# Kernel tuning notes

Measured on AMD Instinct MI355X. Metric: run time of the kernel, lower is better.

The kernel has to match this reference:

```python
import jax, jax.numpy as jnp
import numpy as np

EPS = 1e-5

def layernorm(x, scale, bias):
    mu = jnp.mean(x, axis=-1, keepdims=True)
    var = jnp.var(x, axis=-1, keepdims=True)
    return (x - mu) * jax.lax.rsqrt(var + EPS) * scale + bias

def setup_inputs() -> dict:
    key = jax.random.key(0)
    ks = jax.random.split(key, 12)
    B, N, c_s, c_z, H = 1, 1024, 768, 128, 12
    sc = 1.0 / np.sqrt(c_s)
    inp = {
        "s": jax.random.normal(ks[0], (B, N, c_s), jnp.float32),
        "z": jax.random.normal(ks[1], (B, N, N, c_z), jnp.float32),
        "mask": jnp.ones((B, N), jnp.float32),
        "norm_s_scale": jnp.ones((c_s,), jnp.float32),
        "norm_s_bias": jnp.zeros((c_s,), jnp.float32),
        "Wq": jax.random.normal(ks[2], (c_s, c_s), jnp.float32) * sc,
        "bq": jax.random.normal(ks[3], (c_s,), jnp.float32) * 0.02,
        "Wk": jax.random.normal(ks[4], (c_s, c_s), jnp.float32) * sc,
        "Wv": jax.random.normal(ks[5], (c_s, c_s), jnp.float32) * sc,
        "Wg": jax.random.normal(ks[6], (c_s, c_s), jnp.float32) * sc,
        "norm_z_scale": jnp.ones((c_z,), jnp.float32),
        "norm_z_bias": jnp.zeros((c_z,), jnp.float32),
        "Wz": jax.random.normal(ks[7], (c_z, H), jnp.float32) / np.sqrt(c_z),
        "Wo": jax.random.normal(ks[8], (c_s, c_s), jnp.float32) * sc,  # zero-init in orig; random for nontrivial test
    }
    return inp

def reference(s, z, mask, norm_s_scale, norm_s_bias, Wq, bq, Wk, Wv, Wg,
              norm_z_scale, norm_z_bias, Wz, Wo):
    B, N, c_s = s.shape
    H = Wz.shape[1]
    D = c_s // H
    INF = 1000000.0
    sn = layernorm(s, norm_s_scale, norm_s_bias)                 # (B,N,c_s)
    q = (sn @ Wq + bq).reshape(B, N, H, D)
    k = (sn @ Wk).reshape(B, N, H, D)
    v = (sn @ Wv).reshape(B, N, H, D)
    g = jax.nn.sigmoid(sn @ Wg)                                  # (B,N,c_s)
    zb = jnp.einsum('bijc,ch->bhij', layernorm(z, norm_z_scale, norm_z_bias), Wz)
    attn = jnp.einsum('bihd,bjhd->bhij', q, k) / np.sqrt(D) + zb
    attn = attn + (1.0 - mask[:, None, None, :]) * -INF
    attn = jax.nn.softmax(attn, axis=-1)
    o = jnp.einsum('bhij,bjhd->bihd', attn, v).reshape(B, N, c_s)
    return (g * o) @ Wo
```

## Files before the change

kernel.cpp:

```cpp
#include <hip/hip_runtime.h>
#include <hip/hip_bf16.h>

#define CS 768
#define NTOK 1024
#define CZ 128
#define NH 12
#define HD 64
#define JC 8
#define SMAX_SHIFT 16.0f

typedef __attribute__((ext_vector_type(8))) short bf16x8;
typedef __attribute__((ext_vector_type(4))) float f32x4;
typedef __attribute__((ext_vector_type(8))) unsigned short ushort8_t;
typedef __attribute__((ext_vector_type(4))) unsigned short ushort4_t;

__device__ inline unsigned short f2bf(float f) {
  __hip_bfloat16 h = __float2bfloat16(f);
  return *reinterpret_cast<unsigned short*>(&h);
}
__device__ inline float bf2f(unsigned short u) {
  union { unsigned int i; float f; } c; c.i = ((unsigned int)u) << 16;
  return c.f;
}
__device__ inline unsigned int cvtpk_bf16(float lo, float hi) {
  unsigned int r;
  asm("v_cvt_pk_bf16_f32 %0, %1, %2" : "=v"(r) : "v"(lo), "v"(hi));
  return r;
}

__global__ __launch_bounds__(256) void prep_kernel(const float* __restrict__ s,
    const float* __restrict__ sc, const float* __restrict__ bi, unsigned short* __restrict__ sn,
    const float* __restrict__ W0, const float* __restrict__ W1, const float* __restrict__ W2,
    const float* __restrict__ W3, const float* __restrict__ W4, unsigned short* __restrict__ wt) {
  __shared__ float tile[64][65];
  int tid = threadIdx.x;
  if (blockIdx.x < NTOK) {
    int row = blockIdx.x;
    const float* x = s + (size_t)row * CS;
    float v0 = x[tid], v1 = x[tid + 256], v2 = x[tid + 512];
    float sum = v0 + v1 + v2;
    float sq  = v0*v0 + v1*v1 + v2*v2;
    for (int off = 1; off < 64; off <<= 1) {
      sum += __shfl_xor(sum, off);
      sq  += __shfl_xor(sq,  off);
    }
    __shared__ float ws1[4], ws2[4];
    if ((tid & 63) == 0) { ws1[tid >> 6] = sum; ws2[tid >> 6] = sq; }
    __syncthreads();
    float S = ws1[0] + ws1[1] + ws1[2] + ws1[3];
    float Q = ws2[0] + ws2[1] + ws2[2] + ws2[3];
    float mu  = S * (1.f / CS);
    float var = Q * (1.f / CS) - mu * mu;
    float rs  = rsqrtf(var + 1e-5f);
    unsigned short* y = sn + (size_t)row * CS;
    y[tid]       = f2bf((v0 - mu) * rs * sc[tid]       + bi[tid]);
    y[tid + 256] = f2bf((v1 - mu) * rs * sc[tid + 256] + bi[tid + 256]);
    y[tid + 512] = f2bf((v2 - mu) * rs * sc[tid + 512] + bi[tid + 512]);
  } else {
    int bz = blockIdx.x - NTOK;
    int w = bz / 144, rem = bz % 144;
    int kt = rem % 12, nt = rem / 12;
    const float* W = w == 0 ? W0 : w == 1 ? W1 : w == 2 ? W2 : w == 3 ? W3 : W4;
    unsigned short* Wt = wt + (size_t)w * CS * CS;
    int k0 = kt * 64, n0 = nt * 64;
    #pragma unroll
    for (int it = 0; it < 4; ++it) {
      int r = (tid >> 4) + it * 16;
      int c = (tid & 15) * 4;
      float4 vv = *(const float4*)(W + (size_t)(k0 + r) * CS + n0 + c);
      tile[r][c] = vv.x; tile[r][c+1] = vv.y; tile[r][c+2] = vv.z; tile[r][c+3] = vv.w;
    }
    __syncthreads();
    #pragma unroll
    for (int it = 0; it < 2; ++it) {
      int idx = tid + it * 256;
      int n = idx >> 3, k8 = (idx & 7) * 8;
      ushort8_t o;
      #pragma unroll
      for (int e = 0; e < 8; ++e) o[e] = f2bf(tile[k8 + e][n]);
      *(ushort8_t*)(Wt + (size_t)(n0 + n) * CS + k0 + k8) = o;
    }
  }
}

__global__ __launch_bounds__(256) void zbqkvg_kernel(const float* __restrict__ z,
    const float* __restrict__ gs, const float* __restrict__ gb,
    const float* __restrict__ Wz, const float* __restrict__ mask, float* __restrict__ zbuf,
    const unsigned short* __restrict__ A, const unsigned short* __restrict__ Wt,
    const float* __restrict__ bq, unsigned short* __restrict__ qb,
    unsigned short* __restrict__ kb, unsigned short* __restrict__ vtb,
    unsigned short* __restrict__ gbuf) {
  __shared__ __align__(16) unsigned short As[64][40];
  __shared__ __align__(16) unsigned short Bs[64][40];
  int tid = threadIdx.x;
  int bq11 = blockIdx.x / 11, br11 = blockIdx.x % 11;
  if (br11 < 8) {
    const int zbid = bq11 * 8 + br11;
    const int lane = tid & 63;
    const int il = lane & 15;
    const int qg = lane >> 4;
    const size_t NPAIR = (size_t)NTOK * NTOK;
    bf16x8 whi[4], wlo[4];
    float bh = 0.f;
    #pragma unroll
    for (int m = 0; m < 4; ++m) {
      union { unsigned short u[8]; bf16x8 v; } hi, lo;
      #pragma unroll
      for (int e = 0; e < 8; ++e) {
        int c = 32 * m + 8 * qg + e;
        float wv = (il < NH) ? Wz[c * NH + il] : 0.f;
        bh = fmaf(gb[c], wv, bh);
        float wp = gs[c] * wv;
        unsigned short h = f2bf(wp);
        hi.u[e] = h;
        lo.u[e] = f2bf(wp - bf2f(h));
      }
      whi[m] = hi.v; wlo[m] = lo.v;
    }
    bh += __shfl_xor(bh, 16);
    bh += __shfl_xor(bh, 32);

    const int wave = zbid * 4 + (tid >> 6);
    const int nWaves = 2048 * 4;
    for (size_t p0 = (size_t)wave * 16; p0 < NPAIR; p0 += (size_t)nWaves * 16) {
      const float* zrow = z + (p0 + il) * CZ;
      float zv[32];
      #pragma unroll
      for (int m = 0; m < 4; ++m) {
        float4 a = *(const float4*)(zrow + 32 * m + 8 * qg);
        float4 b = *(const float4*)(zrow + 32 * m + 8 * qg + 4);
        zv[m*8+0] = a.x; zv[m*8+1] = a.y; zv[m*8+2] = a.z; zv[m*8+3] = a.w;
        zv[m*8+4] = b.x; zv[m*8+5] = b.y; zv[m*8+6] = b.z; zv[m*8+7] = b.w;
      }
      float sum = 0.f, sq = 0.f;
      #pragma unroll
      for (int e = 0; e < 32; ++e) { sum += zv[e]; sq = fmaf(zv[e], zv[e], sq); }
      sum += __shfl_xor(sum, 16); sum += __shfl_xor(sum, 32);
      sq  += __shfl_xor(sq,  16); sq  += __shfl_xor(sq,  32);
      float mu  = sum * (1.f / CZ);
      float var = sq * (1.f / CZ) - mu * mu;
      float rs  = rsqrtf(var + 1e-5f);
      float nmr = -mu * rs;
      f32x4 acc = {};
      #pragma unroll
      for (int m = 0; m < 4; ++m) {
        union { unsigned int u[4]; bf16x8 v; } hi;
        #pragma unroll
        for (int e2 = 0; e2 < 4; ++e2) {
          float n0 = fmaf(zv[m*8+e2*2],     rs, nmr);
          float n1 = fmaf(zv[m*8+e2*2 + 1], rs, nmr);
          hi.u[e2] = cvtpk_bf16(n0, n1);
        }
        acc = __builtin_amdgcn_mfma_f32_16x16x32_bf16(hi.v, whi[m], acc, 0, 0, 0);
        acc = __builtin_amdgcn_mfma_f32_16x16x32_bf16(hi.v, wlo[m], acc, 0, 0, 0);
      }
      if (il < NH) {
        int j0 = (int)(p0 & (NTOK - 1)) + 4 * qg;
        float4 mk = *(const float4*)(mask + j0);
        float4 o;
        o.x = (acc[0] + bh + (1.f - mk.x) * -1000000.0f) * 1.44269504f - SMAX_SHIFT;
        o.y = (acc[1] + bh + (1.f - mk.y) * -1000000.0f) * 1.44269504f - SMAX_SHIFT;
        o.z = (acc[2] + bh + (1.f - mk.z) * -1000000.0f) * 1.44269504f - SMAX_SHIFT;
        o.w = (acc[3] + bh + (1.f - mk.w) * -1000000.0f) * 1.44269504f - SMAX_SHIFT;
        *(float4*)(zbuf + (size_t)il * NPAIR + p0 + 4 * qg) = o;
      }
    }
  } else {
    int bx = bq11 * 3 + (br11 - 8);
    int wid = tid >> 6, lane = tid & 63;
    int lrow = lane & 15, lk8 = (lane >> 4) * 8;
    int row0 = (bx / 48) * 64, col0 = (bx % 48) * 64;
    int ar = tid >> 2, ak = (tid & 3) * 8;
    f32x4 acc[4] = {};
    for (int k0 = 0; k0 < CS; k0 += 32) {
      *(ushort8_t*)&As[ar][ak] = *(const ushort8_t*)(A  + (size_t)(row0 + ar) * CS + k0 + ak);
      *(ushort8_t*)&Bs[ar][ak] = *(const ushort8_t*)(Wt + (size_t)(col0 + ar) * CS + k0 + ak);
      __syncthreads();
      bf16x8 af = *(bf16x8*)&As[wid * 16 + lrow][lk8];
      #pragma unroll
      for (int nb = 0; nb < 4; ++nb) {
        bf16x8 bfr = *(bf16x8*)&Bs[nb * 16 + lrow][lk8];
        acc[nb] = __builtin_amdgcn_mfma_f32_16x16x32_bf16(af, bfr, acc[nb], 0, 0, 0);
      }
      __syncthreads();
    }
    int sect = col0 / CS;
    int ncol0 = col0 - sect * CS;
    int grow0 = row0 + wid * 16 + (lane >> 4) * 4;
    if (sect == 2) {
      int jperm0 = ((grow0 >> 5) << 5) + 8 * (lane >> 4) + 4 * (wid & 1);
      #pragma unroll
      for (int nb = 0; nb < 4; ++nb) {
        int dg = ncol0 + nb * 16 + lrow;
        ushort4_t o;
        #pragma unroll
        for (int r = 0; r < 4; ++r) o[r] = f2bf(acc[nb][r]);
        *(ushort4_t*)(vtb + (size_t)dg * NTOK + jperm0) = o;
      }
    } else {
      unsigned short* dst = sect == 0 ? qb : sect == 1 ? kb : gbuf;
      #pragma unroll
      for (int nb = 0; nb < 4; ++nb) {
        int gcol = ncol0 + nb * 16 + lrow;
        float bv = (sect == 0) ? bq[gcol] : 0.f;
        #pragma unroll
        for (int r = 0; r < 4; ++r) {
          float val = acc[nb][r] + bv;
          if (sect == 3) val = 1.f / (1.f + __expf(-val));
          dst[(size_t)(grow0 + r) * CS + gcol] = f2bf(val);
        }
      }
    }
  }
}

__global__ __launch_bounds__(256) void flash_part(
    const unsigned short* __restrict__ qb, const unsigned short* __restrict__ kb,
    const unsigned short* __restrict__ vtb, const float* __restrict__ zbuf,
    float* __restrict__ Opart, float* __restrict__ lsum) {
  const int h = blockIdx.x;
  const int i0 = blockIdx.y * 64;
  const int jc = blockIdx.z;
  const int w = threadIdx.x >> 6, lane = threadIdx.x & 63;
  const int il = lane & 15, g = lane >> 4;
  const int irow = i0 + w * 16 + il;
  const float QKS = 0.125f * 1.44269504f;

  bf16x8 qf0 = *(const bf16x8*)(qb + (size_t)irow * CS + h * HD + g * 8);
  bf16x8 qf1 = *(const bf16x8*)(qb + (size_t)irow * CS + h * HD + 32 + g * 8);

  f32x4 oacc[4] = {};
  float plocal = 0.f;
  const float* zrow = zbuf + ((size_t)h << 20) + ((size_t)irow << 10);

  const int jlo = jc * (NTOK / JC), jhi = jlo + (NTOK / JC);
  for (int j0 = jlo; j0 < jhi; j0 += 64) {
    f32x4 sacc[4] = {};
    #pragma unroll
    for (int jb = 0; jb < 4; ++jb) {
      const unsigned short* kbase = kb + (size_t)(j0 + jb * 16 + il) * CS + h * HD;
      bf16x8 kf0 = *(const bf16x8*)(kbase + g * 8);
      bf16x8 kf1 = *(const bf16x8*)(kbase + 32 + g * 8);
      sacc[jb] = __builtin_amdgcn_mfma_f32_16x16x32_bf16(kf0, qf0, sacc[jb], 0, 0, 0);
      sacc[jb] = __builtin_amdgcn_mfma_f32_16x16x32_bf16(kf1, qf1, sacc[jb], 0, 0, 0);
    }
    unsigned int c0[4], c1[4];
    #pragma unroll
    for (int jb = 0; jb < 4; ++jb) {
      float4 z4 = *(const float4*)(zrow + j0 + jb * 16 + g * 4);
      float p0 = exp2f(fmaf(sacc[jb][0], QKS, z4.x));
      float p1 = exp2f(fmaf(sacc[jb][1], QKS, z4.y));
      float p2 = exp2f(fmaf(sacc[jb][2], QKS, z4.z));
      float p3 = exp2f(fmaf(sacc[jb][3], QKS, z4.w));
      plocal += (p0 + p1) + (p2 + p3);
      c0[jb] = cvtpk_bf16(p0, p1);
      c1[jb] = cvtpk_bf16(p2, p3);
    }
    #pragma unroll
    for (int js = 0; js < 2; ++js) {
      union { unsigned int u[4]; bf16x8 v; } pb;
      pb.u[0] = c0[2*js];
      pb.u[1] = c1[2*js];
      pb.u[2] = c0[2*js + 1];
      pb.u[3] = c1[2*js + 1];
      #pragma unroll
      for (int db = 0; db < 4; ++db) {
        bf16x8 vf = *(const bf16x8*)(vtb + (size_t)(h * HD + db * 16 + il) * NTOK + j0 + js * 32 + g * 8);
        oacc[db] = __builtin_amdgcn_mfma_f32_16x16x32_bf16(vf, pb.v, oacc[db], 0, 0, 0);
      }
    }
  }
  plocal += __shfl_xor(plocal, 16);
  plocal += __shfl_xor(plocal, 32);
  float* obase = Opart + ((size_t)(jc * NH + h) << 16) + ((size_t)irow << 6);
  #pragma unroll
  for (int db = 0; db < 4; ++db)
    *(float4*)(obase + db * 16 + g * 4) = *(float4*)&oacc[db];
  if (g == 0)
    lsum[((jc * NH + h) << 10) + irow] = plocal;
}

__global__ __launch_bounds__(256) void combine_kernel(const float* __restrict__ Opart,
    const float* __restrict__ lsum, const unsigned short* __restrict__ gbuf,
    unsigned short* __restrict__ gob) {
  int t = threadIdx.x;
  int r = blockIdx.x * 4 + (t >> 6);
  int h = r >> 10, i = r & (NTOK - 1), d = t & 63;
  float ltot = 0.f;
  #pragma unroll
  for (int c = 0; c < JC; ++c) ltot += lsum[((c * NH + h) << 10) + i];
  float o = 0.f;
  #pragma unroll
  for (int c = 0; c < JC; ++c)
    o += Opart[((size_t)(c * NH + h) << 16) + ((size_t)i << 6) + d];
  float inv = 1.f / ltot;
  size_t off = (size_t)i * CS + h * HD + d;
  gob[off] = f2bf(o * inv * bf2f(gbuf[off]));
}

__global__ __launch_bounds__(256) void out_gemm(const unsigned short* __restrict__ A,
    const unsigned short* __restrict__ Bt, float* __restrict__ C) {
  __shared__ __align__(16) unsigned short As[64][40];
  __shared__ __align__(16) unsigned short Bs[64][40];
  int tid = threadIdx.x;
  int wid = tid >> 6, lane = tid & 63;
  int lrow = lane & 15, lk8 = (lane >> 4) * 8;
  int row0 = blockIdx.y * 64, col0 = blockIdx.x * 64;
  int ar = tid >> 2, ak = (tid & 3) * 8;
  f32x4 acc[4] = {};
  for (int k0 = 0; k0 < CS; k0 += 32) {
    *(ushort8_t*)&As[ar][ak] = *(const ushort8_t*)(A  + (size_t)(row0 + ar) * CS + k0 + ak);
    *(ushort8_t*)&Bs[ar][ak] = *(const ushort8_t*)(Bt + (size_t)(col0 + ar) * CS + k0 + ak);
    __syncthreads();
    bf16x8 af = *(bf16x8*)&As[wid * 16 + lrow][lk8];
    #pragma unroll
    for (int nb = 0; nb < 4; ++nb) {
      bf16x8 bfr = *(bf16x8*)&Bs[nb * 16 + lrow][lk8];
      acc[nb] = __builtin_amdgcn_mfma_f32_16x16x32_bf16(af, bfr, acc[nb], 0, 0, 0);
    }
    __syncthreads();
  }
  #pragma unroll
  for (int nb = 0; nb < 4; ++nb) {
    int gcol = col0 + nb * 16 + lrow;
    #pragma unroll
    for (int r = 0; r < 4; ++r) {
      int grow = row0 + wid * 16 + (lane >> 4) * 4 + r;
      C[(size_t)grow * CS + gcol] = acc[nb][r];
    }
  }
}

extern "C" void kernel_launch(void* const* d_in, const int* in_sizes, int n_in,
                              void* d_out, int out_size, void* d_ws, size_t ws_size,
                              hipStream_t stream) {
  const float* s    = (const float*)d_in[0];
  const float* z    = (const float*)d_in[1];
  const float* mask = (const float*)d_in[2];
  const float* nss  = (const float*)d_in[3];
  const float* nsb  = (const float*)d_in[4];
  const float* Wq   = (const float*)d_in[5];
  const float* bq   = (const float*)d_in[6];
  const float* Wk   = (const float*)d_in[7];
  const float* Wv   = (const float*)d_in[8];
  const float* Wg   = (const float*)d_in[9];
  const float* nzs  = (const float*)d_in[10];
  const float* nzb  = (const float*)d_in[11];
  const float* Wz   = (const float*)d_in[12];
  const float* Wo   = (const float*)d_in[13];
  float* out = (float*)d_out;

  const size_t SN = (size_t)NTOK * CS;
  const size_t NPAIR = (size_t)NTOK * NTOK;
  const size_t WSZ = (size_t)CS * CS;

  float* zbuf  = (float*)d_ws;
  float* Opart = zbuf + NH * NPAIR;
  float* lsum  = Opart + (size_t)JC * NH * NTOK * HD;
  unsigned short* sn  = (unsigned short*)(lsum + (size_t)JC * NH * NTOK);
  unsigned short* qb  = sn  + SN;
  unsigned short* kb  = qb  + SN;
  unsigned short* vtb = kb  + SN;
  unsigned short* gbuf= vtb + SN;
  unsigned short* gob = gbuf+ SN;
  unsigned short* wt  = gob + SN;

  prep_kernel<<<NTOK + 720, 256, 0, stream>>>(s, nss, nsb, sn, Wq, Wk, Wv, Wg, Wo, wt);
  zbqkvg_kernel<<<2816, 256, 0, stream>>>(z, nzs, nzb, Wz, mask, zbuf,
                                          sn, wt, bq, qb, kb, vtb, gbuf);
  flash_part<<<dim3(NH, 16, JC), 256, 0, stream>>>(qb, kb, vtb, zbuf, Opart, lsum);
  combine_kernel<<<NH * NTOK / 4, 256, 0, stream>>>(Opart, lsum, gbuf, gob);
  out_gemm<<<dim3(12, 16), 256, 0, stream>>>(gob, wt + 4 * WSZ, out);
}
```

Before: 203.0 us.

## Fuse z layernorm pair bias into flash attention via fp16 shared memory tiles

Splits the QKVG GEMM back into its own kernel and fuses the z-projection (layernorm plus Wz MFMA) into the flash-attention kernel. Each block computes the pair bias for a 16x128 tile of all 12 heads into fp16 shared memory, then runs attention over that tile. This removes the 48MB fp32 zbuf write and re-read through HBM. In exchange the bias is stored in fp16, which loses precision, and the fused kernel runs on only 512 blocks with about 52KB of LDS each, so occupancy is lower. Overlap between the z pass and the GEMM in the old combined launch is also lost.

Result: faster. 176.1 us (median of 3 runs) (-13.3%).

```diff
diff --git a/kernel.cpp b/kernel.cpp
--- a/kernel.cpp
+++ b/kernel.cpp
@@ -1,5 +1,6 @@
 #include <hip/hip_runtime.h>
 #include <hip/hip_bf16.h>
+#include <hip/hip_fp16.h>
 
 #define CS 768
 #define NTOK 1024
@@ -7,7 +8,7 @@
 #define NH 12
 #define HD 64
 #define JC 8
-#define SMAX_SHIFT 16.0f
+#define ZHS 2184
 
 typedef __attribute__((ext_vector_type(8))) short bf16x8;
 typedef __attribute__((ext_vector_type(4))) float f32x4;
@@ -25,6 +26,11 @@
 __device__ inline unsigned int cvtpk_bf16(float lo, float hi) {
   unsigned int r;
   asm("v_cvt_pk_bf16_f32 %0, %1, %2" : "=v"(r) : "v"(lo), "v"(hi));
+  return r;
+}
+__device__ inline unsigned int cvtpk_f16(float lo, float hi) {
+  unsigned int r;
+  asm("v_cvt_pkrtz_f16_f32 %0, %1, %2" : "=v"(r) : "v"(lo), "v"(hi));
   return r;
 }
 
@@ -83,201 +89,201 @@
   }
 }
 
-__global__ __launch_bounds__(256) void zbqkvg_kernel(const float* __restrict__ z,
-    const float* __restrict__ gs, const float* __restrict__ gb,
-    const float* __restrict__ Wz, const float* __restrict__ mask, float* __restrict__ zbuf,
-    const unsigned short* __restrict__ A, const unsigned short* __restrict__ Wt,
-    const float* __restrict__ bq, unsigned short* __restrict__ qb,
-    unsigned short* __restrict__ kb, unsigned short* __restrict__ vtb,
-    unsigned short* __restrict__ gbuf) {
+__global__ __launch_bounds__(256) void qkvg_gemm(const unsigned short* __restrict__ A,
+    const unsigned short* __restrict__ Wt, const float* __restrict__ bq,
+    unsigned short* __restrict__ qb, unsigned short* __restrict__ kb,
+    unsigned short* __restrict__ vtb, unsigned short* __restrict__ gbuf) {
   __shared__ __align__(16) unsigned short As[64][40];
   __shared__ __align__(16) unsigned short Bs[64][40];
   int tid = threadIdx.x;
-  int bq11 = blockIdx.x / 11, br11 = blockIdx.x % 11;
-  if (br11 < 8) {
-    const int zbid = bq11 * 8 + br11;
-    const int lane = tid & 63;
-    const int il = lane & 15;
-    const int qg = lane >> 4;
-    const size_t NPAIR = (size_t)NTOK * NTOK;
-    bf16x8 whi[4], wlo[4];
-    float bh = 0.f;
+  int wid = tid >> 6, lane = tid & 63;
+  int lrow = lane & 15, lk8 = (lane >> 4) * 8;
+  int row0 = blockIdx.y * 64, col0 = blockIdx.x * 64;
+  int ar = tid >> 2, ak = (tid & 3) * 8;
+  f32x4 acc[4] = {};
+  for (int k0 = 0; k0 < CS; k0 += 32) {
+    *(ushort8_t*)&As[ar][ak] = *(const ushort8_t*)(A  + (size_t)(row0 + ar) * CS + k0 + ak);
+    *(ushort8_t*)&Bs[ar][ak] = *(const ushort8_t*)(Wt + (size_t)(col0 + ar) * CS + k0 + ak);
+    __syncthreads();
+    bf16x8 af = *(bf16x8*)&As[wid * 16 + lrow][lk8];
+    #pragma unroll
+    for (int nb = 0; nb < 4; ++nb) {
+      bf16x8 bfr = *(bf16x8*)&Bs[nb * 16 + lrow][lk8];
+      acc[nb] = __builtin_amdgcn_mfma_f32_16x16x32_bf16(af, bfr, acc[nb], 0, 0, 0);
+    }
+    __syncthreads();
+  }
+  int sect = col0 / CS;
+  int ncol0 = col0 - sect * CS;
+  int grow0 = row0 + wid * 16 + (lane >> 4) * 4;
+  if (sect == 2) {
+    int jperm0 = ((grow0 >> 5) << 5) + 8 * (lane >> 4) + 4 * (wid & 1);
+    #pragma unroll
+    for (int nb = 0; nb < 4; ++nb) {
+      int dg = ncol0 + nb * 16 + lrow;
+      ushort4_t o;
+      #pragma unroll
+      for (int r = 0; r < 4; ++r) o[r] = f2bf(acc[nb][r]);
+      *(ushort4_t*)(vtb + (size_t)dg * NTOK + jperm0) = o;
+    }
+  } else {
+    unsigned short* dst = sect == 0 ? qb : sect == 1 ? kb : gbuf;
+    #pragma unroll
+    for (int nb = 0; nb < 4; ++nb) {
+      int gcol = ncol0 + nb * 16 + lrow;
+      float bv = (sect == 0) ? bq[gcol] : 0.f;
+      #pragma unroll
+      for (int r = 0; r < 4; ++r) {
+        float val = acc[nb][r] + bv;
+        if (sect == 3) val = 1.f / (1.f + __expf(-val));
+        dst[(size_t)(grow0 + r) * CS + gcol] = f2bf(val);
+      }
+    }
+  }
+}
+
+__global__ __launch_bounds__(256) void zbflash_kernel(const float* __restrict__ z,
+    const float* __restrict__ gs, const float* __restrict__ gb,
+    const float* __restrict__ Wz, const float* __restrict__ mask,
+    const unsigned short* __restrict__ qb, const unsigned short* __restrict__ kb,
+    const unsigned short* __restrict__ vtb,
+    float* __restrict__ Opart, float* __restrict__ lsum) {
+  __shared__ __half zs[NH * ZHS];
+  const int i0 = blockIdx.x * 16;
+  const int jc = blockIdx.y;
+  const int j0 = jc * 128;
+  const int tid = threadIdx.x;
+  const int w = tid >> 6, lane = tid & 63;
+  const int il = lane & 15, qg = lane >> 4;
+  const float QKS = 0.125f * 1.44269504f;
+
+  bf16x8 whi[4], wlo[4];
+  float bh = 0.f;
+  #pragma unroll
+  for (int m = 0; m < 4; ++m) {
+    union { unsigned short u[8]; bf16x8 v; } hi, lo;
+    #pragma unroll
+    for (int e = 0; e < 8; ++e) {
+      int c = 32 * m + 8 * qg + e;
+      float wv = (il < NH) ? Wz[c * NH + il] : 0.f;
+      bh = fmaf(gb[c], wv, bh);
+      float wp = gs[c] * wv;
+      unsigned short h = f2bf(wp);
+      hi.u[e] = h;
+      lo.u[e] = f2bf(wp - bf2f(h));
+    }
+    whi[m] = hi.v; wlo[m] = lo.v;
+  }
+  bh += __shfl_xor(bh, 16);
+  bh += __shfl_xor(bh, 32);
+
+  for (int it = 0; it < 32; ++it) {
+    int group = w * 32 + it;
+    int i_local = group >> 3;
+    int jseg = group & 7;
+    const float* zrow = z + ((size_t)(i0 + i_local) * NTOK + j0 + jseg * 16 + il) * CZ;
+    float zv[32];
     #pragma unroll
     for (int m = 0; m < 4; ++m) {
-      union { unsigned short u[8]; bf16x8 v; } hi, lo;
-      #pragma unroll
-      for (int e = 0; e < 8; ++e) {
-        int c = 32 * m + 8 * qg + e;
-        float wv = (il < NH) ? Wz[c * NH + il] : 0.f;
-        bh = fmaf(gb[c], wv, bh);
-        float wp = gs[c] * wv;
-        unsigned short h = f2bf(wp);
-        hi.u[e] = h;
-        lo.u[e] = f2bf(wp - bf2f(h));
-      }
-      whi[m] = hi.v; wlo[m] = lo.v;
-    }
-    bh += __shfl_xor(bh, 16);
-    bh += __shfl_xor(bh, 32);
-
-    const int wave = zbid * 4 + (tid >> 6);
-    const int nWaves = 2048 * 4;
-    for (size_t p0 = (size_t)wave * 16; p0 < NPAIR; p0 += (size_t)nWaves * 16) {
-      const float* zrow = z + (p0 + il) * CZ;
-      float zv[32];
-      #pragma unroll
-      for (int m = 0; m < 4; ++m) {
-        float4 a = *(const float4*)(zrow + 32 * m + 8 * qg);
-        float4 b = *(const float4*)(zrow + 32 * m + 8 * qg + 4);
-        zv[m*8+0] = a.x; zv[m*8+1] = a.y; zv[m*8+2] = a.z; zv[m*8+3] = a.w;
-        zv[m*8+4] = b.x; zv[m*8+5] = b.y; zv[m*8+6] = b.z; zv[m*8+7] = b.w;
-      }
-      float sum = 0.f, sq = 0.f;
-      #pragma unroll
-      for (int e = 0; e < 32; ++e) { sum += zv[e]; sq = fmaf(zv[e], zv[e], sq); }
-      sum += __shfl_xor(sum, 16); sum += __shfl_xor(sum, 32);
-      sq  += __shfl_xor(sq,  16); sq  += __shfl_xor(sq,  32);
-      float mu  = sum * (1.f / CZ);
-      float var = sq * (1.f / CZ) - mu * mu;
-      float rs  = rsqrtf(var + 1e-5f);
-      float nmr = -mu * rs;
-      f32x4 acc = {};
-      #pragma unroll
-      for (int m = 0; m < 4; ++m) {
-        union { unsigned int u[4]; bf16x8 v; } hi;
+      float4 a = *(const float4*)(zrow + 32 * m + 8 * qg);
+      float4 b = *(const float4*)(zrow + 32 * m + 8 * qg + 4);
+      zv[m*8+0] = a.x; zv[m*8+1] = a.y; zv[m*8+2] = a.z; zv[m*8+3] = a.w;
+      zv[m*8+4] = b.x; zv[m*8+5] = b.y; zv[m*8+6] = b.z; zv[m*8+7] = b.w;
+    }
+    float sum = 0.f, sq = 0.f;
+    #pragma unroll
+    for (int e = 0; e < 32; ++e) { sum += zv[e]; sq = fmaf(zv[e], zv[e], sq); }
+    sum += __shfl_xor(sum, 16); sum += __shfl_xor(sum, 32);
+    sq  += __shfl_xor(sq,  16); sq  += __shfl_xor(sq,  32);
+    float mu  = sum * (1.f / CZ);
+    float var = sq * (1.f / CZ) - mu * mu;
+    float rs  = rsqrtf(var + 1e-5f);
+    float nmr = -mu * rs;
+    f32x4 acc = {};
+    #pragma unroll
+    for (int m = 0; m < 4; ++m) {
+      union { unsigned int u[4]; bf16x8 v; } hi;
+      #pragma unroll
+      for (int e2 = 0; e2 < 4; ++e2) {
+        float n0 = fmaf(zv[m*8+e2*2],     rs, nmr);
+        float n1 = fmaf(zv[m*8+e2*2 + 1], rs, nmr);
+        hi.u[e2] = cvtpk_bf16(n0, n1);
+      }
+      acc = __builtin_amdgcn_mfma_f32_16x16x32_bf16(hi.v, whi[m], acc, 0, 0, 0);
+      acc = __builtin_amdgcn_mfma_f32_16x16x32_bf16(hi.v, wlo[m], acc, 0, 0, 0);
+    }
+    if (il < NH) {
+      int jl = jseg * 16 + 4 * qg;
+      float4 mk = *(const float4*)(mask + j0 + jl);
+      float o0 = (acc[0] + bh + (1.f - mk.x) * -1000000.0f) * 1.44269504f - 16.f;
+      float o1 = (acc[1] + bh + (1.f - mk.y) * -1000000.0f) * 1.44269504f - 16.f;
+      float o2 = (acc[2] + bh + (1.f - mk.z) * -1000000.0f) * 1.44269504f - 16.f;
+      float o3 = (acc[3] + bh + (1.f - mk.w) * -1000000.0f) * 1.44269504f - 16.f;
+      unsigned int p01 = cvtpk_f16(o0, o1);
+      unsigned int p23 = cvtpk_f16(o2, o3);
+      *(uint2*)(zs + il * ZHS + i_local * 136 + jl) = make_uint2(p01, p23);
+    }
+  }
+  __syncthreads();
+
+  const int irow = i0 + il;
+  for (int hh = 0; hh < 3; ++hh) {
+    const int h = w * 3 + hh;
+    bf16x8 qf0 = *(const bf16x8*)(qb + (size_t)irow * CS + h * HD + qg * 8);
+    bf16x8 qf1 = *(const bf16x8*)(qb + (size_t)irow * CS + h * HD + 32 + qg * 8);
+    const __half* zh = zs + h * ZHS + il * 136;
+    f32x4 oacc[4] = {};
+    float plocal = 0.f;
+    #pragma unroll
+    for (int jt = 0; jt < 2; ++jt) {
+      int jb0 = j0 + jt * 64;
+      f32x4 sacc[4] = {};
+      #pragma unroll
+      for (int jb = 0; jb < 4; ++jb) {
+        const unsigned short* kbase = kb + (size_t)(jb0 + jb * 16 + il) * CS + h * HD;
+        bf16x8 kf0 = *(const bf16x8*)(kbase + qg * 8);
+        bf16x8 kf1 = *(const bf16x8*)(kbase + 32 + qg * 8);
+        sacc[jb] = __builtin_amdgcn_mfma_f32_16x16x32_bf16(kf0, qf0, sacc[jb], 0, 0, 0);
+        sacc[jb] = __builtin_amdgcn_mfma_f32_16x16x32_bf16(kf1, qf1, sacc[jb], 0, 0, 0);
+      }
+      unsigned int c0[4], c1[4];
+      #pragma unroll
+      for (int jb = 0; jb < 4; ++jb) {
+        uint2 zr = *(const uint2*)(zh + jt * 64 + jb * 16 + qg * 4);
+        const __half2* hz = (const __half2*)&zr;
+        float z0 = __low2float(hz[0]), z1 = __high2float(hz[0]);
+        float z2 = __low2float(hz[1]), z3 = __high2float(hz[1]);
+        float p0 = exp2f(fmaf(sacc[jb][0], QKS, z0));
+        float p1 = exp2f(fmaf(sacc[jb][1], QKS, z1));
+        float p2 = exp2f(fmaf(sacc[jb][2], QKS, z2));
+        float p3 = exp2f(fmaf(sacc[jb][3], QKS, z3));
+        plocal += (p0 + p1) + (p2 + p3);
+        c0[jb] = cvtpk_bf16(p0, p1);
+        c1[jb] = cvtpk_bf16(p2, p3);
+      }
+      #pragma unroll
+      for (int js = 0; js < 2; ++js) {
+        union { unsigned int u[4]; bf16x8 v; } pb;
+        pb.u[0] = c0[2*js];
+        pb.u[1] = c1[2*js];
+        pb.u[2] = c0[2*js + 1];
+        pb.u[3] = c1[2*js + 1];
         #pragma unroll
-        for (int e2 = 0; e2 < 4; ++e2) {
-          float n0 = fmaf(zv[m*8+e2*2],     rs, nmr);
-          float n1 = fmaf(zv[m*8+e2*2 + 1], rs, nmr);
-          hi.u[e2] = cvtpk_bf16(n0, n1);
+        for (int db = 0; db < 4; ++db) {
+          bf16x8 vf = *(const bf16x8*)(vtb + (size_t)(h * HD + db * 16 + il) * NTOK + jb0 + js * 32 + qg * 8);
+          oacc[db] = __builtin_amdgcn_mfma_f32_16x16x32_bf16(vf, pb.v, oacc[db], 0, 0, 0);
         }
-        acc = __builtin_amdgcn_mfma_f32_16x16x32_bf16(hi.v, whi[m], acc, 0, 0, 0);
-        acc = __builtin_amdgcn_mfma_f32_16x16x32_bf16(hi.v, wlo[m], acc, 0, 0, 0);
-      }
-      if (il < NH) {
-        int j0 = (int)(p0 & (NTOK - 1)) + 4 * qg;
-        float4 mk = *(const float4*)(mask + j0);
-        float4 o;
-        o.x = (acc[0] + bh + (1.f - mk.x) * -1000000.0f) * 1.44269504f - SMAX_SHIFT;
-        o.y = (acc[1] + bh + (1.f - mk.y) * -1000000.0f) * 1.44269504f - SMAX_SHIFT;
-        o.z = (acc[2] + bh + (1.f - mk.z) * -1000000.0f) * 1.44269504f - SMAX_SHIFT;
-        o.w = (acc[3] + bh + (1.f - mk.w) * -1000000.0f) * 1.44269504f - SMAX_SHIFT;
-        *(float4*)(zbuf + (size_t)il * NPAIR + p0 + 4 * qg) = o;
-      }
-    }
-  } else {
-    int bx = bq11 * 3 + (br11 - 8);
-    int wid = tid >> 6, lane = tid & 63;
-    int lrow = lane & 15, lk8 = (lane >> 4) * 8;
-    int row0 = (bx / 48) * 64, col0 = (bx % 48) * 64;
-    int ar = tid >> 2, ak = (tid & 3) * 8;
-    f32x4 acc[4] = {};
-    for (int k0 = 0; k0 < CS; k0 += 32) {
-      *(ushort8_t*)&As[ar][ak] = *(const ushort8_t*)(A  + (size_t)(row0 + ar) * CS + k0 + ak);
-      *(ushort8_t*)&Bs[ar][ak] = *(const ushort8_t*)(Wt + (size_t)(col0 + ar) * CS + k0 + ak);
-      __syncthreads();
-      bf16x8 af = *(bf16x8*)&As[wid * 16 + lrow][lk8];
-      #pragma unroll
-      for (int nb = 0; nb < 4; ++nb) {
-        bf16x8 bfr = *(bf16x8*)&Bs[nb * 16 + lrow][lk8];
-        acc[nb] = __builtin_amdgcn_mfma_f32_16x16x32_bf16(af, bfr, acc[nb], 0, 0, 0);
-      }
-      __syncthreads();
-    }
-    int sect = col0 / CS;
-    int ncol0 = col0 - sect * CS;
-    int grow0 = row0 + wid * 16 + (lane >> 4) * 4;
-    if (sect == 2) {
-      int jperm0 = ((grow0 >> 5) << 5) + 8 * (lane >> 4) + 4 * (wid & 1);
-      #pragma unroll
-      for (int nb = 0; nb < 4; ++nb) {
-        int dg = ncol0 + nb * 16 + lrow;
-        ushort4_t o;
-        #pragma unroll
-        for (int r = 0; r < 4; ++r) o[r] = f2bf(acc[nb][r]);
-        *(ushort4_t*)(vtb + (size_t)dg * NTOK + jperm0) = o;
-      }
-    } else {
-      unsigned short* dst = sect == 0 ? qb : sect == 1 ? kb : gbuf;
-      #pragma unroll
-      for (int nb = 0; nb < 4; ++nb) {
-        int gcol = ncol0 + nb * 16 + lrow;
-        float bv = (sect == 0) ? bq[gcol] : 0.f;
-        #pragma unroll
-        for (int r = 0; r < 4; ++r) {
-          float val = acc[nb][r] + bv;
-          if (sect == 3) val = 1.f / (1.f + __expf(-val));
-          dst[(size_t)(grow0 + r) * CS + gcol] = f2bf(val);
-        }
-      }
-    }
-  }
-}
-
-__global__ __launch_bounds__(256) void flash_part(
-    const unsigned short* __restrict__ qb, const unsigned short* __restrict__ kb,
-    const unsigned short* __restrict__ vtb, const float* __restrict__ zbuf,
-    float* __restrict__ Opart, float* __restrict__ lsum) {
-  const int h = blockIdx.x;
-  const int i0 = blockIdx.y * 64;
-  const int jc = blockIdx.z;
-  const int w = threadIdx.x >> 6, lane = threadIdx.x & 63;
-  const int il = lane & 15, g = lane >> 4;
-  const int irow = i0 + w * 16 + il;
-  const float QKS = 0.125f * 1.44269504f;
-
-  bf16x8 qf0 = *(const bf16x8*)(qb + (size_t)irow * CS + h * HD + g * 8);
-  bf16x8 qf1 = *(const bf16x8*)(qb + (size_t)irow * CS + h * HD + 32 + g * 8);
-
-  f32x4 oacc[4] = {};
-  float plocal = 0.f;
-  const float* zrow = zbuf + ((size_t)h << 20) + ((size_t)irow << 10);
-
-  const int jlo = jc * (NTOK / JC), jhi = jlo + (NTOK / JC);
-  for (int j0 = jlo; j0 < jhi; j0 += 64) {
-    f32x4 sacc[4] = {};
-    #pragma unroll
-    for (int jb = 0; jb < 4; ++jb) {
-      const unsigned short* kbase = kb + (size_t)(j0 + jb * 16 + il) * CS + h * HD;
-      bf16x8 kf0 = *(const bf16x8*)(kbase + g * 8);
-      bf16x8 kf1 = *(const bf16x8*)(kbase + 32 + g * 8);
-      sacc[jb] = __builtin_amdgcn_mfma_f32_16x16x32_bf16(kf0, qf0, sacc[jb], 0, 0, 0);
-      sacc[jb] = __builtin_amdgcn_mfma_f32_16x16x32_bf16(kf1, qf1, sacc[jb], 0, 0, 0);
-    }
-    unsigned int c0[4], c1[4];
-    #pragma unroll
-    for (int jb = 0; jb < 4; ++jb) {
-      float4 z4 = *(const float4*)(zrow + j0 + jb * 16 + g * 4);
-      float p0 = exp2f(fmaf(sacc[jb][0], QKS, z4.x));
-      float p1 = exp2f(fmaf(sacc[jb][1], QKS, z4.y));
-      float p2 = exp2f(fmaf(sacc[jb][2], QKS, z4.z));
-      float p3 = exp2f(fmaf(sacc[jb][3], QKS, z4.w));
-      plocal += (p0 + p1) + (p2 + p3);
-      c0[jb] = cvtpk_bf16(p0, p1);
-      c1[jb] = cvtpk_bf16(p2, p3);
-    }
-    #pragma unroll
-    for (int js = 0; js < 2; ++js) {
-      union { unsigned int u[4]; bf16x8 v; } pb;
-      pb.u[0] = c0[2*js];
-      pb.u[1] = c1[2*js];
-      pb.u[2] = c0[2*js + 1];
-      pb.u[3] = c1[2*js + 1];
-      #pragma unroll
-      for (int db = 0; db < 4; ++db) {
-        bf16x8 vf = *(const bf16x8*)(vtb + (size_t)(h * HD + db * 16 + il) * NTOK + j0 + js * 32 + g * 8);
-        oacc[db] = __builtin_amdgcn_mfma_f32_16x16x32_bf16(vf, pb.v, oacc[db], 0, 0, 0);
-      }
-    }
-  }
-  plocal += __shfl_xor(plocal, 16);
-  plocal += __shfl_xor(plocal, 32);
-  float* obase = Opart + ((size_t)(jc * NH + h) << 16) + ((size_t)irow << 6);
-  #pragma unroll
-  for (int db = 0; db < 4; ++db)
-    *(float4*)(obase + db * 16 + g * 4) = *(float4*)&oacc[db];
-  if (g == 0)
-    lsum[((jc * NH + h) << 10) + irow] = plocal;
+      }
+    }
+    plocal += __shfl_xor(plocal, 16);
+    plocal += __shfl_xor(plocal, 32);
+    float* obase = Opart + ((size_t)(jc * NH + h) << 16) + ((size_t)irow << 6);
+    #pragma unroll
+    for (int db = 0; db < 4; ++db)
+      *(float4*)(obase + db * 16 + qg * 4) = *(float4*)&oacc[db];
+    if (qg == 0)
+      lsum[((jc * NH + h) << 10) + irow] = plocal;
+  }
 }
 
 __global__ __launch_bounds__(256) void combine_kernel(const float* __restrict__ Opart,
@@ -351,11 +357,9 @@
   float* out = (float*)d_out;
 
   const size_t SN = (size_t)NTOK * CS;
-  const size_t NPAIR = (size_t)NTOK * NTOK;
   const size_t WSZ = (size_t)CS * CS;
 
-  float* zbuf  = (float*)d_ws;
-  float* Opart = zbuf + NH * NPAIR;
+  float* Opart = (float*)d_ws;
   float* lsum  = Opart + (size_t)JC * NH * NTOK * HD;
   unsigned short* sn  = (unsigned short*)(lsum + (size_t)JC * NH * NTOK);
   unsigned short* qb  = sn  + SN;
@@ -366,9 +370,9 @@
   unsigned short* wt  = gob + SN;
 
   prep_kernel<<<NTOK + 720, 256, 0, stream>>>(s, nss, nsb, sn, Wq, Wk, Wv, Wg, Wo, wt);
-  zbqkvg_kernel<<<2816, 256, 0, stream>>>(z, nzs, nzb, Wz, mask, zbuf,
-                                          sn, wt, bq, qb, kb, vtb, gbuf);
-  flash_part<<<dim3(NH, 16, JC), 256, 0, stream>>>(qb, kb, vtb, zbuf, Opart, lsum);
+  qkvg_gemm<<<dim3(48, 16), 256, 0, stream>>>(sn, wt, bq, qb, kb, vtb, gbuf);
+  zbflash_kernel<<<dim3(64, JC), 256, 0, stream>>>(z, nzs, nzb, Wz, mask,
+                                                   qb, kb, vtb, Opart, lsum);
   combine_kernel<<<NH * NTOK / 4, 256, 0, stream>>>(Opart, lsum, gbuf, gob);
   out_gemm<<<dim3(12, 16), 256, 0, stream>>>(gob, wt + 4 * WSZ, out);
 }
```
